# Performance work log

Measured on AMD Instinct MI355X. Metric: run time of the kernel, lower is better.

## Reference

```python
import jax, jax.numpy as jnp
import numpy as np

N = 100_000      # nodes
E = 1_600_000    # edges (before self loops)
IN = 128         # in_dim
HID = 64         # hidden_dim (per head)
HEADS = 2
NEG_SLOPE = 0.2  # PyG GATConv default negative_slope


def setup_inputs() -> dict:
    key = jax.random.key(0)
    k = jax.random.split(key, 6)
    x = jax.random.normal(k[0], (N, IN), jnp.float32)
    edge_index = jax.random.randint(k[1], (2, E), 0, N, dtype=jnp.int64)
    # GATConv linear (no bias in lin, bias added after aggregation in PyG)
    W = jax.random.normal(k[2], (IN, HEADS * HID), jnp.float32) * (1.0 / np.sqrt(IN))
    att_src = jax.random.normal(k[3], (HEADS, HID), jnp.float32) * 0.1
    att_dst = jax.random.normal(k[4], (HEADS, HID), jnp.float32) * 0.1
    bias = jnp.zeros((HEADS * HID,), jnp.float32)
    prelu_w = jnp.full((HEADS * HID,), 0.25, jnp.float32)  # nn.PReLU default init
    return {"x": x, "edge_index": edge_index, "W": W, "att_src": att_src,
            "att_dst": att_dst, "bias": bias, "prelu_w": prelu_w}


def reference(x, edge_index, W, att_src, att_dst, bias, prelu_w):
    n = x.shape[0]
    h = (x @ W).reshape(n, HEADS, HID)                 # [N,H,C]
    a_s = jnp.einsum('nhc,hc->nh', h, att_src)         # [N,H]
    a_d = jnp.einsum('nhc,hc->nh', h, att_dst)         # [N,H]
    # add self loops (PyG default add_self_loops=True)
    loops = jnp.arange(n, dtype=edge_index.dtype)
    src = jnp.concatenate([edge_index[0], loops])      # [Et]
    dst = jnp.concatenate([edge_index[1], loops])      # [Et]
    logits = a_s[src] + a_d[dst]                       # [Et,H]
    logits = jnp.where(logits >= 0, logits, NEG_SLOPE * logits)  # LeakyReLU
    # segment softmax over destination neighborhoods
    m = jax.ops.segment_max(logits, dst, num_segments=n)         # [N,H]
    e = jnp.exp(logits - m[dst])
    s = jax.ops.segment_sum(e, dst, num_segments=n)              # [N,H]
    alpha = e / (s[dst] + 1e-16)                                 # [Et,H]
    # (attention dropout p=0.2 is identity in eval mode)
    msg = h[src] * alpha[..., None]                    # [Et,H,C]
    out = jax.ops.segment_sum(msg, dst, num_segments=n).reshape(n, HEADS * HID)
    out = out + bias
    # PReLU with per-channel weight
    return jnp.where(out >= 0, out, prelu_w * out)
```

## Files before the change

kernel.cpp:

```cpp
#include <hip/hip_runtime.h>
#include <cstdint>
#include <cstddef>

#define NEG_SLOPE 0.2f
#define BSH 9
#define BNODES 512
#define CAP 12288

typedef __attribute__((ext_vector_type(8))) short short8v;
typedef __attribute__((ext_vector_type(4))) float f32x4;

__device__ __forceinline__ uint32_t bf16pair(float a, float b) {
    uint32_t ua = __float_as_uint(a), ub = __float_as_uint(b);
    ua = (ua + 0x7fffu + ((ua >> 16) & 1u)) >> 16;
    ub = (ub + 0x7fffu + ((ub >> 16) & 1u)) >> 16;
    return ua | (ub << 16);
}
__device__ __forceinline__ uint16_t rne16(float f) {
    uint32_t u = __float_as_uint(f);
    return (uint16_t)((u + 0x7fffu + ((u >> 16) & 1u)) >> 16);
}
__device__ __forceinline__ float bflo(uint32_t u) { return __uint_as_float(u << 16); }
__device__ __forceinline__ float bfhi(uint32_t u) { return __uint_as_float(u & 0xffff0000u); }

__global__ __launch_bounds__(256, 3) void gemm_att(
    const float* __restrict__ x, const float* __restrict__ W,
    const float* __restrict__ att_src, const float* __restrict__ att_dst,
    uint32_t* __restrict__ hb, float* __restrict__ a_s, float* __restrict__ a_d,
    int n)
{
    constexpr int PW = 136;
    __shared__ unsigned short Wt[128 * PW];
    __shared__ unsigned short Hs[4][16 * PW];
    const int tid  = threadIdx.x;
    const int w    = tid >> 6;
    const int lane = tid & 63;
    const int cl   = lane & 15;
    const int gq   = lane >> 4;
    const int base = blockIdx.x * 64;

    const float4* W4 = (const float4*)W;
#pragma unroll
    for (int i = 0; i < 16; ++i) {
        int idx = tid + i * 256;
        int k = idx >> 5, c0 = (idx & 31) * 4;
        float4 v = W4[idx];
        Wt[(c0 + 0) * PW + k] = rne16(v.x);
        Wt[(c0 + 1) * PW + k] = rne16(v.y);
        Wt[(c0 + 2) * PW + k] = rne16(v.z);
        Wt[(c0 + 3) * PW + k] = rne16(v.w);
    }

    float asr[8], adr[8];
#pragma unroll
    for (int t = 0; t < 8; ++t) {
        asr[t] = att_src[t * 16 + cl];
        adr[t] = att_dst[t * 16 + cl];
    }
    __syncthreads();

    const int rowg = base + w * 16 + cl;
    const int rowc = rowg < n ? rowg : (n - 1);
    const float4* xp = (const float4*)(x + (size_t)rowc * 128);

    f32x4 acc[8];
#pragma unroll
    for (int t = 0; t < 8; ++t) acc[t] = (f32x4){0.f, 0.f, 0.f, 0.f};

#pragma unroll
    for (int s = 0; s < 4; ++s) {
        int kq = s * 8 + gq * 2;
        float4 f0 = xp[kq], f1 = xp[kq + 1];
        union { short8v v; uint32_t d[4]; } A;
        A.d[0] = bf16pair(f0.x, f0.y);
        A.d[1] = bf16pair(f0.z, f0.w);
        A.d[2] = bf16pair(f1.x, f1.y);
        A.d[3] = bf16pair(f1.z, f1.w);
#pragma unroll
        for (int t = 0; t < 8; ++t) {
            union { short8v v; uint4 q; } B;
            B.q = *(const uint4*)&Wt[(t * 16 + cl) * PW + s * 32 + gq * 8];
            acc[t] = __builtin_amdgcn_mfma_f32_16x16x32_bf16(A.v, B.v, acc[t], 0, 0, 0);
        }
    }

    float ps0[4], ps1[4], pd0[4], pd1[4];
#pragma unroll
    for (int r = 0; r < 4; ++r) { ps0[r] = ps1[r] = pd0[r] = pd1[r] = 0.f; }
#pragma unroll
    for (int t = 0; t < 8; ++t) {
#pragma unroll
        for (int r = 0; r < 4; ++r) {
            float v = acc[t][r];
            if (t < 4) { ps0[r] = fmaf(v, asr[t], ps0[r]); pd0[r] = fmaf(v, adr[t], pd0[r]); }
            else       { ps1[r] = fmaf(v, asr[t], ps1[r]); pd1[r] = fmaf(v, adr[t], pd1[r]); }
        }
    }
#pragma unroll
    for (int off = 1; off < 16; off <<= 1) {
#pragma unroll
        for (int r = 0; r < 4; ++r) {
            ps0[r] += __shfl_xor(ps0[r], off);
            ps1[r] += __shfl_xor(ps1[r], off);
            pd0[r] += __shfl_xor(pd0[r], off);
            pd1[r] += __shfl_xor(pd1[r], off);
        }
    }
    if (cl == 0) {
#pragma unroll
        for (int r = 0; r < 4; ++r) {
            int rg = base + w * 16 + gq * 4 + r;
            if (rg < n) {
                a_s[rg * 2 + 0] = ps0[r]; a_s[rg * 2 + 1] = ps1[r];
                a_d[rg * 2 + 0] = pd0[r]; a_d[rg * 2 + 1] = pd1[r];
            }
        }
    }

#pragma unroll
    for (int t = 0; t < 8; ++t) {
#pragma unroll
        for (int r = 0; r < 4; ++r) {
            int row = gq * 4 + r;
            Hs[w][row * PW + t * 16 + cl] = rne16(acc[t][r]);
        }
    }
    __syncthreads();
#pragma unroll
    for (int q = 0; q < 4; ++q) {
        int row = q * 4 + gq;
        int cu  = 4 * cl;
        uint4 v = *(const uint4*)&Hs[w][row * PW + cu * 2];
        int rg = base + w * 16 + row;
        if (rg < n) *(uint4*)&hb[(size_t)rg * 64 + cu] = v;
    }
}

__global__ void zero_gcur(int* gcur, int nb) {
    if ((int)threadIdx.x < nb) gcur[threadIdx.x] = 0;
}

__global__ __launch_bounds__(256) void bucket_scatter(
    const int* __restrict__ src, const int* __restrict__ dst,
    int* __restrict__ gcur, uint32_t* __restrict__ pairs, int e, int nb)
{
    __shared__ int histL[256];
    __shared__ int gbaseL[256];
    const int tid = threadIdx.x;
    const int t0  = blockIdx.x * 4096;

    if (tid < nb) histL[tid] = 0;
    __syncthreads();

    int      myb[16];
    int      myslot[16];
    uint32_t mypk[16];
#pragma unroll 16
    for (int k = 0; k < 16; ++k) {
        int i = t0 + tid + k * 256;
        if (i < e) {
            int s = src[i], d = dst[i];
            int b = d >> BSH;
            myb[k]    = b;
            mypk[k]   = (uint32_t)s | ((uint32_t)(d & (BNODES - 1)) << 17);
            myslot[k] = atomicAdd(&histL[b], 1);
        } else myb[k] = -1;
    }
    __syncthreads();
    if (tid < nb) {
        int c = histL[tid];
        gbaseL[tid] = c ? atomicAdd(&gcur[tid], c) : 0;
    }
    __syncthreads();
#pragma unroll 16
    for (int k = 0; k < 16; ++k) {
        if (myb[k] >= 0) {
            int p = gbaseL[myb[k]] + myslot[k];
            if (p < CAP) pairs[(size_t)myb[k] * CAP + p] = mypk[k];
        }
    }
}

__global__ __launch_bounds__(256) void bucket_scan(
    const int* __restrict__ gcur, int* __restrict__ bbase, int* __restrict__ bcnt,
    int nb, int n)
{
    __shared__ int sh[256];
    const int tid = threadIdx.x;
    int nodes = 0, c = 0;
    if (tid < nb) {
        nodes = min(BNODES, n - tid * BNODES);
        c = min(gcur[tid], CAP);
    }
    int tot = c + nodes;
    sh[tid] = tot;
    __syncthreads();
    for (int off = 1; off < 256; off <<= 1) {
        int t = (tid >= off) ? sh[tid - off] : 0;
        __syncthreads();
        sh[tid] += t;
        __syncthreads();
    }
    if (tid < nb) { bbase[tid] = sh[tid] - tot; bcnt[tid] = c; }
}

__global__ __launch_bounds__(512) void build_csr(
    const uint32_t* __restrict__ pairs, const int* __restrict__ bbase,
    const int* __restrict__ bcnt, int* __restrict__ row_ptr,
    int* __restrict__ cnt, int* __restrict__ col, int n)
{
    __shared__ uint32_t pl[CAP];
    __shared__ int degL[BNODES], curL[BNODES], scanL[BNODES];
    const int b = blockIdx.x, tid = threadIdx.x;
    const int nbase = b * BNODES;
    const int nodes = min(BNODES, n - nbase);
    const int C     = bcnt[b];
    const int base  = bbase[b];

    degL[tid] = 1;
    __syncthreads();
    for (int i = tid; i < C; i += 512) {
        uint32_t p = pairs[(size_t)b * CAP + i];
        pl[i] = p;
        atomicAdd(&degL[p >> 17], 1);
    }
    __syncthreads();
    int v = (tid < nodes) ? degL[tid] : 0;
    scanL[tid] = v;
    __syncthreads();
    for (int off = 1; off < 512; off <<= 1) {
        int t = (tid >= off) ? scanL[tid - off] : 0;
        __syncthreads();
        scanL[tid] += t;
        __syncthreads();
    }
    if (tid < nodes) {
        int exc = scanL[tid] - v;
        int g   = nbase + tid;
        row_ptr[g] = base + exc;
        cnt[g]     = v;
        col[base + exc] = g;
        curL[tid]  = exc + 1;
    }
    __syncthreads();
    for (int i = tid; i < C; i += 512) {
        uint32_t p  = pl[i];
        int dl  = p >> 17;
        int s   = p & 0x1FFFF;
        int pos = atomicAdd(&curL[dl], 1);
        col[base + pos] = s;
    }
}

__global__ __launch_bounds__(256) void attn_agg(
    const uint32_t* __restrict__ hb, const float* __restrict__ a_s,
    const float* __restrict__ a_d, const int* __restrict__ row_ptr,
    const int* __restrict__ cnt, const int* __restrict__ col,
    const float* __restrict__ bias, const float* __restrict__ prelu_w,
    float* __restrict__ out, int n)
{
    const int gw   = (blockIdx.x * blockDim.x + threadIdx.x) >> 6;
    const int lane = threadIdx.x & 63;
    if (gw >= n) return;
    const int start = row_ptr[gw];
    const int deg   = cnt[gw];
    const float2 ad = ((const float2*)a_d)[gw];

    float accL, accH;

    if (deg <= 64) {
        int   sv = 0;
        float l0 = -1e30f, l1 = -1e30f;
        const bool act = lane < deg;
        if (act) {
            sv = col[start + lane];
            float2 as = ((const float2*)a_s)[sv];
            l0 = as.x + ad.x; l0 = l0 >= 0.f ? l0 : NEG_SLOPE * l0;
            l1 = as.y + ad.y; l1 = l1 >= 0.f ? l1 : NEG_SLOPE * l1;
        }
        float m0 = l0, m1 = l1;
#pragma unroll
        for (int off = 32; off > 0; off >>= 1) {
            m0 = fmaxf(m0, __shfl_xor(m0, off));
            m1 = fmaxf(m1, __shfl_xor(m1, off));
        }
        float e0 = act ? __expf(l0 - m0) : 0.f;
        float e1 = act ? __expf(l1 - m1) : 0.f;
        float s0 = e0, s1 = e1;
#pragma unroll
        for (int off = 32; off > 0; off >>= 1) {
            s0 += __shfl_xor(s0, off);
            s1 += __shfl_xor(s1, off);
        }
        float al0 = e0 * (1.f / (s0 + 1e-16f));
        float al1 = e1 * (1.f / (s1 + 1e-16f));

        const int g = lane >> 4, r = lane & 15;
        float acc[8];
#pragma unroll
        for (int q = 0; q < 8; ++q) acc[q] = 0.f;

        const int iters = (deg + 3) >> 2;
        for (int jj = 0; jj < iters; ++jj) {
            const int j = jj * 4 + g;
            int   s  = __shfl(sv, j);
            float A0 = __shfl(al0, j);
            float A1 = __shfl(al1, j);
            if (j < deg) {
                const uint32_t* hp = hb + (size_t)s * 64;
                uint32_t u0 = hp[r], u1 = hp[16 + r], u2 = hp[32 + r], u3 = hp[48 + r];
                acc[0] = fmaf(A0, bflo(u0), acc[0]);
                acc[1] = fmaf(A0, bfhi(u0), acc[1]);
                acc[2] = fmaf(A0, bflo(u1), acc[2]);
                acc[3] = fmaf(A0, bfhi(u1), acc[3]);
                acc[4] = fmaf(A1, bflo(u2), acc[4]);
                acc[5] = fmaf(A1, bfhi(u2), acc[5]);
                acc[6] = fmaf(A1, bflo(u3), acc[6]);
                acc[7] = fmaf(A1, bfhi(u3), acc[7]);
            }
        }
#pragma unroll
        for (int q = 0; q < 8; ++q) {
            acc[q] += __shfl_xor(acc[q], 16);
            acc[q] += __shfl_xor(acc[q], 32);
        }
        accL = (g == 0) ? acc[0] : (g == 1) ? acc[2] : (g == 2) ? acc[4] : acc[6];
        accH = (g == 0) ? acc[1] : (g == 1) ? acc[3] : (g == 2) ? acc[5] : acc[7];
    } else {
        float m0 = -1e30f, m1 = -1e30f;
        for (int t = lane; t < deg; t += 64) {
            int s = col[start + t];
            float2 as = ((const float2*)a_s)[s];
            float l0 = as.x + ad.x; l0 = l0 >= 0.f ? l0 : NEG_SLOPE * l0;
            float l1 = as.y + ad.y; l1 = l1 >= 0.f ? l1 : NEG_SLOPE * l1;
            m0 = fmaxf(m0, l0); m1 = fmaxf(m1, l1);
        }
#pragma unroll
        for (int off = 32; off > 0; off >>= 1) {
            m0 = fmaxf(m0, __shfl_xor(m0, off));
            m1 = fmaxf(m1, __shfl_xor(m1, off));
        }
        float s0 = 0.f, s1 = 0.f;
        for (int t = lane; t < deg; t += 64) {
            int s = col[start + t];
            float2 as = ((const float2*)a_s)[s];
            float l0 = as.x + ad.x; l0 = l0 >= 0.f ? l0 : NEG_SLOPE * l0;
            float l1 = as.y + ad.y; l1 = l1 >= 0.f ? l1 : NEG_SLOPE * l1;
            s0 += __expf(l0 - m0); s1 += __expf(l1 - m1);
        }
#pragma unroll
        for (int off = 32; off > 0; off >>= 1) {
            s0 += __shfl_xor(s0, off);
            s1 += __shfl_xor(s1, off);
        }
        const float inv0 = 1.f / (s0 + 1e-16f);
        const float inv1 = 1.f / (s1 + 1e-16f);
        accL = 0.f; accH = 0.f;
        for (int t0 = 0; t0 < deg; t0 += 64) {
            int tt = t0 + lane;
            float al0 = 0.f, al1 = 0.f; int sv = 0;
            if (tt < deg) {
                sv = col[start + tt];
                float2 as = ((const float2*)a_s)[sv];
                float l0 = as.x + ad.x; l0 = l0 >= 0.f ? l0 : NEG_SLOPE * l0;
                float l1 = as.y + ad.y; l1 = l1 >= 0.f ? l1 : NEG_SLOPE * l1;
                al0 = __expf(l0 - m0) * inv0;
                al1 = __expf(l1 - m1) * inv1;
            }
            int kmax = min(64, deg - t0);
            for (int j = 0; j < kmax; ++j) {
                int   s  = __shfl(sv, j);
                float A0 = __shfl(al0, j);
                float A1 = __shfl(al1, j);
                float A  = (lane < 32) ? A0 : A1;
                uint32_t u = hb[(size_t)s * 64 + lane];
                accL = fmaf(A, bflo(u), accL);
                accH = fmaf(A, bfhi(u), accH);
            }
        }
    }

    float2 bz = ((const float2*)bias)[lane];
    float2 pw = ((const float2*)prelu_w)[lane];
    float o0 = accL + bz.x, o1 = accH + bz.y;
    o0 = o0 >= 0.f ? o0 : pw.x * o0;
    o1 = o1 >= 0.f ? o1 : pw.y * o1;
    float2 rr; rr.x = o0; rr.y = o1;
    ((float2*)out)[(size_t)gw * 64 + lane] = rr;
}

extern "C" void kernel_launch(void* const* d_in, const int* in_sizes, int n_in,
                              void* d_out, int out_size, void* d_ws, size_t ws_size,
                              hipStream_t stream)
{
    const float* x        = (const float*)d_in[0];
    const int*   ei       = (const int*)d_in[1];
    const float* W        = (const float*)d_in[2];
    const float* att_src  = (const float*)d_in[3];
    const float* att_dst  = (const float*)d_in[4];
    const float* bias     = (const float*)d_in[5];
    const float* prelu_w  = (const float*)d_in[6];
    float* out = (float*)d_out;

    const int n = in_sizes[0] / 128;
    const int e = in_sizes[1] / 2;
    const int* srcp = ei;
    const int* dstp = ei + e;
    const int nb = (n + BNODES - 1) / BNODES;

    uint32_t* hb   = (uint32_t*)d_ws;
    float*    a_s  = (float*)(hb + (size_t)n * 64);
    float*    a_d  = a_s + (size_t)n * 2;
    int*      gcur = (int*)(a_d + (size_t)n * 2);
    int*      bbase= gcur + nb;
    int*      bcnt = bbase + nb;
    int*      row_ptr = bcnt + nb;
    int*      cnt  = row_ptr + n;
    uint32_t* pairs= (uint32_t*)(cnt + n);
    int*      col  = (int*)(pairs + (size_t)nb * CAP);

    gemm_att<<<(n + 63) / 64, 256, 0, stream>>>(x, W, att_src, att_dst,
                                                hb, a_s, a_d, n);
    zero_gcur<<<1, 256, 0, stream>>>(gcur, nb);
    bucket_scatter<<<(e + 4095) / 4096, 256, 0, stream>>>(srcp, dstp, gcur, pairs, e, nb);
    bucket_scan<<<1, 256, 0, stream>>>(gcur, bbase, bcnt, nb, n);
    build_csr<<<nb, 512, 0, stream>>>(pairs, bbase, bcnt, row_ptr, cnt, col, n);
    attn_agg<<<(n + 3) / 4, 256, 0, stream>>>(hb, a_s, a_d, row_ptr, cnt, col,
                                              bias, prelu_w, out, n);
}
```

Measured before the change: 159.3 us.

## Precompute edge softmax weights during CSR build, vectorize aggregation loads

Moves the edge-logit exp and per-destination sum into build_csr. Each edge's unnormalized exp weight is stored as fp16 next to col, and per-node inverse sums go into a separate array. attn_agg then reads precomputed weights instead of recomputing logits, the max and the sum per node, and the small-degree path loads h rows with 16-byte vector loads and stores float4 outputs. It drops the max subtraction, so large logits could overflow exp or lose precision in fp16. It also adds shared-memory float atomics and an extra per-edge write.

```diff
diff --git a/kernel.cpp b/kernel.cpp
--- a/kernel.cpp
+++ b/kernel.cpp
@@ -1,4 +1,5 @@
 #include <hip/hip_runtime.h>
+#include <hip/hip_fp16.h>
 #include <cstdint>
 #include <cstddef>
 
@@ -22,6 +23,10 @@
 }
 __device__ __forceinline__ float bflo(uint32_t u) { return __uint_as_float(u << 16); }
 __device__ __forceinline__ float bfhi(uint32_t u) { return __uint_as_float(u & 0xffff0000u); }
+__device__ __forceinline__ uint32_t packf16(float a, float b) {
+    __half2 h = __floats2half2_rn(a, b);
+    return *reinterpret_cast<uint32_t*>(&h);
+}
 
 __global__ __launch_bounds__(256, 3) void gemm_att(
     const float* __restrict__ x, const float* __restrict__ W,
@@ -206,11 +211,15 @@
 
 __global__ __launch_bounds__(512) void build_csr(
     const uint32_t* __restrict__ pairs, const int* __restrict__ bbase,
-    const int* __restrict__ bcnt, int* __restrict__ row_ptr,
-    int* __restrict__ cnt, int* __restrict__ col, int n)
+    const int* __restrict__ bcnt, const float* __restrict__ a_s,
+    const float* __restrict__ a_d,
+    int* __restrict__ row_ptr, int* __restrict__ cnt, int* __restrict__ col,
+    uint32_t* __restrict__ alph, float2* __restrict__ invs, int n)
 {
     __shared__ uint32_t pl[CAP];
     __shared__ int degL[BNODES], curL[BNODES], scanL[BNODES];
+    __shared__ float sumL[BNODES * 2];
+    __shared__ float adL[BNODES * 2];
     const int b = blockIdx.x, tid = threadIdx.x;
     const int nbase = b * BNODES;
     const int nodes = min(BNODES, n - nbase);
@@ -218,6 +227,18 @@
     const int base  = bbase[b];
 
     degL[tid] = 1;
+    float es0 = 0.f, es1 = 0.f;
+    if (tid < nodes) {
+        int g = nbase + tid;
+        float2 ad = ((const float2*)a_d)[g];
+        adL[2 * tid]     = ad.x;
+        adL[2 * tid + 1] = ad.y;
+        float2 as = ((const float2*)a_s)[g];
+        float l0 = as.x + ad.x; l0 = l0 >= 0.f ? l0 : NEG_SLOPE * l0;
+        float l1 = as.y + ad.y; l1 = l1 >= 0.f ? l1 : NEG_SLOPE * l1;
+        es0 = __expf(l0); es1 = __expf(l1);
+        sumL[2 * tid] = es0; sumL[2 * tid + 1] = es1;
+    }
     __syncthreads();
     for (int i = tid; i < C; i += 512) {
         uint32_t p = pairs[(size_t)b * CAP + i];
@@ -239,7 +260,8 @@
         int g   = nbase + tid;
         row_ptr[g] = base + exc;
         cnt[g]     = v;
-        col[base + exc] = g;
+        col[base + exc]  = g;
+        alph[base + exc] = packf16(es0, es1);
         curL[tid]  = exc + 1;
     }
     __syncthreads();
@@ -247,14 +269,28 @@
         uint32_t p  = pl[i];
         int dl  = p >> 17;
         int s   = p & 0x1FFFF;
+        float2 as = ((const float2*)a_s)[s];
+        float l0 = as.x + adL[2 * dl];     l0 = l0 >= 0.f ? l0 : NEG_SLOPE * l0;
+        float l1 = as.y + adL[2 * dl + 1]; l1 = l1 >= 0.f ? l1 : NEG_SLOPE * l1;
+        float e0 = __expf(l0), e1 = __expf(l1);
         int pos = atomicAdd(&curL[dl], 1);
-        col[base + pos] = s;
+        col[base + pos]  = s;
+        alph[base + pos] = packf16(e0, e1);
+        atomicAdd(&sumL[2 * dl],     e0);
+        atomicAdd(&sumL[2 * dl + 1], e1);
+    }
+    __syncthreads();
+    if (tid < nodes) {
+        float2 iv;
+        iv.x = 1.f / (sumL[2 * tid]     + 1e-16f);
+        iv.y = 1.f / (sumL[2 * tid + 1] + 1e-16f);
+        invs[nbase + tid] = iv;
     }
 }
 
 __global__ __launch_bounds__(256) void attn_agg(
-    const uint32_t* __restrict__ hb, const float* __restrict__ a_s,
-    const float* __restrict__ a_d, const int* __restrict__ row_ptr,
+    const uint32_t* __restrict__ hb, const uint32_t* __restrict__ alph,
+    const float2* __restrict__ invs, const int* __restrict__ row_ptr,
     const int* __restrict__ cnt, const int* __restrict__ col,
     const float* __restrict__ bias, const float* __restrict__ prelu_w,
     float* __restrict__ out, int n)
@@ -264,59 +300,40 @@
     if (gw >= n) return;
     const int start = row_ptr[gw];
     const int deg   = cnt[gw];
-    const float2 ad = ((const float2*)a_d)[gw];
-
-    float accL, accH;
+    const float2 inv = invs[gw];
 
     if (deg <= 64) {
-        int   sv = 0;
-        float l0 = -1e30f, l1 = -1e30f;
-        const bool act = lane < deg;
-        if (act) {
+        int sv = 0; float al0 = 0.f, al1 = 0.f;
+        if (lane < deg) {
             sv = col[start + lane];
-            float2 as = ((const float2*)a_s)[sv];
-            l0 = as.x + ad.x; l0 = l0 >= 0.f ? l0 : NEG_SLOPE * l0;
-            l1 = as.y + ad.y; l1 = l1 >= 0.f ? l1 : NEG_SLOPE * l1;
-        }
-        float m0 = l0, m1 = l1;
-#pragma unroll
-        for (int off = 32; off > 0; off >>= 1) {
-            m0 = fmaxf(m0, __shfl_xor(m0, off));
-            m1 = fmaxf(m1, __shfl_xor(m1, off));
-        }
-        float e0 = act ? __expf(l0 - m0) : 0.f;
-        float e1 = act ? __expf(l1 - m1) : 0.f;
-        float s0 = e0, s1 = e1;
-#pragma unroll
-        for (int off = 32; off > 0; off >>= 1) {
-            s0 += __shfl_xor(s0, off);
-            s1 += __shfl_xor(s1, off);
-        }
-        float al0 = e0 * (1.f / (s0 + 1e-16f));
-        float al1 = e1 * (1.f / (s1 + 1e-16f));
-
+            uint32_t ea = alph[start + lane];
+            __half2 h2 = *reinterpret_cast<__half2*>(&ea);
+            al0 = __half2float(__low2half(h2))  * inv.x;
+            al1 = __half2float(__high2half(h2)) * inv.y;
+        }
         const int g = lane >> 4, r = lane & 15;
         float acc[8];
 #pragma unroll
         for (int q = 0; q < 8; ++q) acc[q] = 0.f;
 
+        const uint4* hb4 = (const uint4*)hb;
         const int iters = (deg + 3) >> 2;
         for (int jj = 0; jj < iters; ++jj) {
             const int j = jj * 4 + g;
             int   s  = __shfl(sv, j);
             float A0 = __shfl(al0, j);
             float A1 = __shfl(al1, j);
+            float A  = (r < 8) ? A0 : A1;
             if (j < deg) {
-                const uint32_t* hp = hb + (size_t)s * 64;
-                uint32_t u0 = hp[r], u1 = hp[16 + r], u2 = hp[32 + r], u3 = hp[48 + r];
-                acc[0] = fmaf(A0, bflo(u0), acc[0]);
-                acc[1] = fmaf(A0, bfhi(u0), acc[1]);
-                acc[2] = fmaf(A0, bflo(u1), acc[2]);
-                acc[3] = fmaf(A0, bfhi(u1), acc[3]);
-                acc[4] = fmaf(A1, bflo(u2), acc[4]);
-                acc[5] = fmaf(A1, bfhi(u2), acc[5]);
-                acc[6] = fmaf(A1, bflo(u3), acc[6]);
-                acc[7] = fmaf(A1, bfhi(u3), acc[7]);
+                uint4 q = hb4[(size_t)s * 16 + r];
+                acc[0] = fmaf(A, bflo(q.x), acc[0]);
+                acc[1] = fmaf(A, bfhi(q.x), acc[1]);
+                acc[2] = fmaf(A, bflo(q.y), acc[2]);
+                acc[3] = fmaf(A, bfhi(q.y), acc[3]);
+                acc[4] = fmaf(A, bflo(q.z), acc[4]);
+                acc[5] = fmaf(A, bfhi(q.z), acc[5]);
+                acc[6] = fmaf(A, bflo(q.w), acc[6]);
+                acc[7] = fmaf(A, bfhi(q.w), acc[7]);
             }
         }
 #pragma unroll
@@ -324,48 +341,34 @@
             acc[q] += __shfl_xor(acc[q], 16);
             acc[q] += __shfl_xor(acc[q], 32);
         }
-        accL = (g == 0) ? acc[0] : (g == 1) ? acc[2] : (g == 2) ? acc[4] : acc[6];
-        accH = (g == 0) ? acc[1] : (g == 1) ? acc[3] : (g == 2) ? acc[5] : acc[7];
+        if (lane < 16) {
+            float4 b0 = ((const float4*)bias)[lane * 2];
+            float4 b1 = ((const float4*)bias)[lane * 2 + 1];
+            float4 p0 = ((const float4*)prelu_w)[lane * 2];
+            float4 p1 = ((const float4*)prelu_w)[lane * 2 + 1];
+            float4 w0, w1;
+            w0.x = acc[0] + b0.x; w0.x = w0.x >= 0.f ? w0.x : p0.x * w0.x;
+            w0.y = acc[1] + b0.y; w0.y = w0.y >= 0.f ? w0.y : p0.y * w0.y;
+            w0.z = acc[2] + b0.z; w0.z = w0.z >= 0.f ? w0.z : p0.z * w0.z;
+            w0.w = acc[3] + b0.w; w0.w = w0.w >= 0.f ? w0.w : p0.w * w0.w;
+            w1.x = acc[4] + b1.x; w1.x = w1.x >= 0.f ? w1.x : p1.x * w1.x;
+            w1.y = acc[5] + b1.y; w1.y = w1.y >= 0.f ? w1.y : p1.y * w1.y;
+            w1.z = acc[6] + b1.z; w1.z = w1.z >= 0.f ? w1.z : p1.z * w1.z;
+            w1.w = acc[7] + b1.w; w1.w = w1.w >= 0.f ? w1.w : p1.w * w1.w;
+            ((float4*)out)[(size_t)gw * 32 + lane * 2]     = w0;
+            ((float4*)out)[(size_t)gw * 32 + lane * 2 + 1] = w1;
+        }
     } else {
-        float m0 = -1e30f, m1 = -1e30f;
-        for (int t = lane; t < deg; t += 64) {
-            int s = col[start + t];
-            float2 as = ((const float2*)a_s)[s];
-            float l0 = as.x + ad.x; l0 = l0 >= 0.f ? l0 : NEG_SLOPE * l0;
-            float l1 = as.y + ad.y; l1 = l1 >= 0.f ? l1 : NEG_SLOPE * l1;
-            m0 = fmaxf(m0, l0); m1 = fmaxf(m1, l1);
-        }
-#pragma unroll
-        for (int off = 32; off > 0; off >>= 1) {
-            m0 = fmaxf(m0, __shfl_xor(m0, off));
-            m1 = fmaxf(m1, __shfl_xor(m1, off));
-        }
-        float s0 = 0.f, s1 = 0.f;
-        for (int t = lane; t < deg; t += 64) {
-            int s = col[start + t];
-            float2 as = ((const float2*)a_s)[s];
-            float l0 = as.x + ad.x; l0 = l0 >= 0.f ? l0 : NEG_SLOPE * l0;
-            float l1 = as.y + ad.y; l1 = l1 >= 0.f ? l1 : NEG_SLOPE * l1;
-            s0 += __expf(l0 - m0); s1 += __expf(l1 - m1);
-        }
-#pragma unroll
-        for (int off = 32; off > 0; off >>= 1) {
-            s0 += __shfl_xor(s0, off);
-            s1 += __shfl_xor(s1, off);
-        }
-        const float inv0 = 1.f / (s0 + 1e-16f);
-        const float inv1 = 1.f / (s1 + 1e-16f);
-        accL = 0.f; accH = 0.f;
+        float accL = 0.f, accH = 0.f;
         for (int t0 = 0; t0 < deg; t0 += 64) {
             int tt = t0 + lane;
-            float al0 = 0.f, al1 = 0.f; int sv = 0;
+            int sv = 0; float al0 = 0.f, al1 = 0.f;
             if (tt < deg) {
                 sv = col[start + tt];
-                float2 as = ((const float2*)a_s)[sv];
-                float l0 = as.x + ad.x; l0 = l0 >= 0.f ? l0 : NEG_SLOPE * l0;
-                float l1 = as.y + ad.y; l1 = l1 >= 0.f ? l1 : NEG_SLOPE * l1;
-                al0 = __expf(l0 - m0) * inv0;
-                al1 = __expf(l1 - m1) * inv1;
+                uint32_t ea = alph[start + tt];
+                __half2 h2 = *reinterpret_cast<__half2*>(&ea);
+                al0 = __half2float(__low2half(h2))  * inv.x;
+                al1 = __half2float(__high2half(h2)) * inv.y;
             }
             int kmax = min(64, deg - t0);
             for (int j = 0; j < kmax; ++j) {
@@ -378,15 +381,14 @@
                 accH = fmaf(A, bfhi(u), accH);
             }
         }
-    }
-
-    float2 bz = ((const float2*)bias)[lane];
-    float2 pw = ((const float2*)prelu_w)[lane];
-    float o0 = accL + bz.x, o1 = accH + bz.y;
-    o0 = o0 >= 0.f ? o0 : pw.x * o0;
-    o1 = o1 >= 0.f ? o1 : pw.y * o1;
-    float2 rr; rr.x = o0; rr.y = o1;
-    ((float2*)out)[(size_t)gw * 64 + lane] = rr;
+        float2 bz = ((const float2*)bias)[lane];
+        float2 pw = ((const float2*)prelu_w)[lane];
+        float o0 = accL + bz.x, o1 = accH + bz.y;
+        o0 = o0 >= 0.f ? o0 : pw.x * o0;
+        o1 = o1 >= 0.f ? o1 : pw.y * o1;
+        float2 rr; rr.x = o0; rr.y = o1;
+        ((float2*)out)[(size_t)gw * 64 + lane] = rr;
+    }
 }
 
 extern "C" void kernel_launch(void* const* d_in, const int* in_sizes, int n_in,
@@ -411,20 +413,23 @@
     uint32_t* hb   = (uint32_t*)d_ws;
     float*    a_s  = (float*)(hb + (size_t)n * 64);
     float*    a_d  = a_s + (size_t)n * 2;
-    int*      gcur = (int*)(a_d + (size_t)n * 2);
+    float2*   invs = (float2*)(a_d + (size_t)n * 2);
+    int*      gcur = (int*)(invs + n);
     int*      bbase= gcur + nb;
     int*      bcnt = bbase + nb;
     int*      row_ptr = bcnt + nb;
     int*      cnt  = row_ptr + n;
     uint32_t* pairs= (uint32_t*)(cnt + n);
     int*      col  = (int*)(pairs + (size_t)nb * CAP);
+    uint32_t* alph = (uint32_t*)(col + (size_t)e + n);
 
     gemm_att<<<(n + 63) / 64, 256, 0, stream>>>(x, W, att_src, att_dst,
                                                 hb, a_s, a_d, n);
     zero_gcur<<<1, 256, 0, stream>>>(gcur, nb);
     bucket_scatter<<<(e + 4095) / 4096, 256, 0, stream>>>(srcp, dstp, gcur, pairs, e, nb);
     bucket_scan<<<1, 256, 0, stream>>>(gcur, bbase, bcnt, nb, n);
-    build_csr<<<nb, 512, 0, stream>>>(pairs, bbase, bcnt, row_ptr, cnt, col, n);
-    attn_agg<<<(n + 3) / 4, 256, 0, stream>>>(hb, a_s, a_d, row_ptr, cnt, col,
+    build_csr<<<nb, 512, 0, stream>>>(pairs, bbase, bcnt, a_s, a_d,
+                                      row_ptr, cnt, col, alph, invs, n);
+    attn_agg<<<(n + 3) / 4, 256, 0, stream>>>(hb, alph, invs, row_ptr, cnt, col,
                                               bias, prelu_w, out, n);
 }
```

Result: slower. 167.5 us (+5.1%).
